# Optimization experiments

Hardware: AMD Instinct MI355X
Metric: run time of the kernel (lower is better)

Reference implementation:

```python
import jax, jax.numpy as jnp
import numpy as np

# Winograd F(2x2, 3x3) transform matrices
_BT = np.array([[1, 0, -1, 0],
                [0, 1,  1, 0],
                [0, -1, 1, 0],
                [0, 1,  0, -1]], dtype=np.float32)
_G = np.array([[1.0, 0.0, 0.0],
               [0.5, 0.5, 0.5],
               [0.5, -0.5, 0.5],
               [0.0, 0.0, 1.0]], dtype=np.float32)
_AT = np.array([[1, 1, 1, 0],
                [0, 1, -1, -1]], dtype=np.float32)


def setup_inputs() -> dict:
    key = jax.random.key(0)
    k1, k2, k3 = jax.random.split(key, 3)
    B, Cin, Cout, H, W = 16, 128, 256, 64, 64
    X = jax.random.normal(k1, (B, Cin, H, W), dtype=jnp.float32)
    # kaiming-uniform-ish scale for a 3x3 conv
    fan_in = Cin * 9
    bound = 1.0 / np.sqrt(fan_in)
    weight = jax.random.uniform(k2, (Cout, Cin, 3, 3), dtype=jnp.float32,
                                minval=-bound * np.sqrt(3.0), maxval=bound * np.sqrt(3.0))
    bias = jax.random.uniform(k3, (Cout,), dtype=jnp.float32, minval=-bound, maxval=bound)
    return {"X": X, "weight": weight, "bias": bias}


def reference(X, weight, bias):
    # Winograd F(2x2,3x3) convolution, stride 1, padding 1 ('same').
    BT = jnp.asarray(_BT, X.dtype)
    G = jnp.asarray(_G, X.dtype)
    AT = jnp.asarray(_AT, X.dtype)
    Bn, C, H, W = X.shape
    K = weight.shape[0]
    tH, tW = H // 2, W // 2  # number of 2x2 output tiles per dim

    xp = jnp.pad(X, ((0, 0), (0, 0), (1, 1), (1, 1)))
    # overlapping 4x4 input tiles with stride 2 -> [B, C, tH, tW, 4, 4]
    rows = (jnp.arange(tH) * 2)[:, None] + jnp.arange(4)[None, :]  # [tH,4]
    cols = (jnp.arange(tW) * 2)[:, None] + jnp.arange(4)[None, :]  # [tW,4]
    d = xp[:, :, rows[:, None, :, None], cols[None, :, None, :]]   # [B,C,tH,tW,4,4]

    # input transform V = B^T d B
    V = jnp.einsum('px,bcijxy,qy->bcijpq', BT, d, BT)
    # filter transform U = G g G^T -> [K,C,4,4]
    U = jnp.einsum('px,kcxy,qy->kcpq', G, weight, G)
    # elementwise product in transform domain, contracted over input channels
    M = jnp.einsum('kcpq,bcijpq->bkijpq', U, V)
    # inverse transform Y = A^T M A -> 2x2 output tiles
    Y = jnp.einsum('px,bkijxy,qy->bkijpq', AT, M, AT)  # [B,K,tH,tW,2,2]

    out = Y.transpose(0, 1, 2, 4, 3, 5).reshape(Bn, K, H, W)
    return out + bias[None, :, None, None]
```

## Files before the change

### kernel.cpp

```cpp
#include <hip/hip_runtime.h>
#include <hip/hip_bf16.h>
#include <cstdint>

#define CIN   128
#define COUT  256
#define BATCH 16
#define HH    64
#define WW    64
#define TH    32
#define TW    32
#define NT    (BATCH*TH*TW)
#define APQ   (COUT*CIN)
#define BPQ   (NT*CIN)

typedef __bf16 bf16x8 __attribute__((ext_vector_type(8)));
typedef float  f32x4  __attribute__((ext_vector_type(4)));

__device__ __forceinline__ void gload16(const void* g, void* l) {
    __builtin_amdgcn_global_load_lds(
        (const __attribute__((address_space(1))) uint32_t*)g,
        (__attribute__((address_space(3))) uint32_t*)l, 16, 0, 0);
}

__global__ __launch_bounds__(256) void wg_wtrans(const float* __restrict__ w,
                                                 __hip_bfloat16* __restrict__ U) {
    int idx = blockIdx.x * 256 + threadIdx.x;
    if (idx >= COUT * CIN) return;
    const float* wp = w + idx * 9;
    float g[3][3];
#pragma unroll
    for (int x = 0; x < 3; x++)
#pragma unroll
        for (int y = 0; y < 3; y++) g[x][y] = wp[x * 3 + y];

    float t[4][3];
#pragma unroll
    for (int y = 0; y < 3; y++) {
        t[0][y] = g[0][y];
        t[1][y] = 0.5f * (g[0][y] + g[1][y] + g[2][y]);
        t[2][y] = 0.5f * (g[0][y] - g[1][y] + g[2][y]);
        t[3][y] = g[2][y];
    }
#pragma unroll
    for (int p = 0; p < 4; p++) {
        float u0 = t[p][0];
        float u1 = 0.5f * (t[p][0] + t[p][1] + t[p][2]);
        float u2 = 0.5f * (t[p][0] - t[p][1] + t[p][2]);
        float u3 = t[p][2];
        U[(p * 4 + 0) * APQ + idx] = __float2bfloat16(u0);
        U[(p * 4 + 1) * APQ + idx] = __float2bfloat16(u1);
        U[(p * 4 + 2) * APQ + idx] = __float2bfloat16(u2);
        U[(p * 4 + 3) * APQ + idx] = __float2bfloat16(u3);
    }
}

__global__ __launch_bounds__(1024) void wg_itrans(const float* __restrict__ X,
                                                  __hip_bfloat16* __restrict__ V) {
    __shared__ float lds[32 * 265];
    const int c0 = blockIdx.x * 32;
    const int i  = blockIdx.y;
    const int b  = blockIdx.z;
    const int tid = threadIdx.x;

    for (int t = tid; t < 32 * 4; t += 1024) {
        int cc = t >> 2, r = t & 3;
        lds[cc * 265 + r * 66 + 0]  = 0.f;
        lds[cc * 265 + r * 66 + 65] = 0.f;
    }
    for (int t = tid; t < 32 * 4 * 64; t += 1024) {
        int x = t & 63, r = (t >> 6) & 3, cc = t >> 8;
        int y = 2 * i - 1 + r;
        float v = 0.f;
        if (y >= 0 && y < HH) v = X[(((b * CIN) + (c0 + cc)) * HH + y) * WW + x];
        lds[cc * 265 + r * 66 + 1 + x] = v;
    }
    __syncthreads();

    const int c = tid & 31;
    const int j = tid >> 5;
    const float* base = &lds[c * 265 + 2 * j];

    float t0[4], t1[4], t2[4], t3[4];
#pragma unroll
    for (int y = 0; y < 4; y++) {
        float a  = base[0 * 66 + y];
        float bb = base[1 * 66 + y];
        float cc = base[2 * 66 + y];
        float dd = base[3 * 66 + y];
        t0[y] = a - cc;
        t1[y] = bb + cc;
        t2[y] = cc - bb;
        t3[y] = bb - dd;
    }
    float vm[4][4];
#pragma unroll
    for (int p = 0; p < 4; p++) {
        const float* tp = (p == 0) ? t0 : (p == 1) ? t1 : (p == 2) ? t2 : t3;
        vm[p][0] = tp[0] - tp[2];
        vm[p][1] = tp[1] + tp[2];
        vm[p][2] = tp[2] - tp[1];
        vm[p][3] = tp[1] - tp[3];
    }

    const int bij = b * (TH * TW) + i * TW + j;
    const int vo  = bij * CIN + (c0 + c);
#pragma unroll
    for (int p = 0; p < 4; p++)
#pragma unroll
        for (int q = 0; q < 4; q++)
            V[(size_t)(p * 4 + q) * BPQ + vo] = __float2bfloat16(vm[p][q]);
}

#define ABYTES 16384
#define BUFSZ  32768

__global__ __launch_bounds__(512, 2) void wg_gemm6(const __hip_bfloat16* __restrict__ U,
                                                   const __hip_bfloat16* __restrict__ V,
                                                   const float* __restrict__ bias,
                                                   float* __restrict__ out) {
    __shared__ char lds[4 * BUFSZ];

    int orig = blockIdx.x;
    int wg   = (orig & 7) * 32 + (orig >> 3);
    const int mt = wg & 1, nt = wg >> 1;
    const int m0 = mt * 128, n0 = nt * 128;

    const int tid  = threadIdx.x;
    const int lane = tid & 63;
    const int wave = tid >> 6;
    const int wm = wave >> 2, wn = wave & 3;

    const __hip_bfloat16* pa[2];
    const __hip_bfloat16* pb[2];
    int ldsA[2], ldsB[2];
#pragma unroll
    for (int ch = 0; ch < 2; ch++) {
        int c = ch * 512 + tid;
        int R = c >> 3;
        int G = (c & 7) ^ (R & 7);
        pa[ch] = U + (m0 + R) * CIN + G * 8;
        pb[ch] = V + (size_t)(n0 + R) * CIN + G * 8;
        ldsA[ch] = c * 16;
        ldsB[ch] = ABYTES + c * 16;
    }

    auto stage = [&](int t, int buf) {
        const int pq = t >> 1;
        const int kb = (t & 1) * 64;
        char* base = lds + buf * BUFSZ;
        gload16(pa[0] + pq * APQ + kb, base + ldsA[0]);
        gload16(pa[1] + pq * APQ + kb, base + ldsA[1]);
        gload16(pb[0] + (size_t)pq * BPQ + kb, base + ldsB[0]);
        gload16(pb[1] + (size_t)pq * BPQ + kb, base + ldsB[1]);
    };

    const int la = lane & 15, hq = lane >> 4, l7 = lane & 7;
    int aoff[2], boff[2];
#pragma unroll
    for (int kk = 0; kk < 2; kk++) {
        int g = (kk * 4 + hq) ^ l7;
        aoff[kk] = (wm * 64 + la) * 128 + (g << 4);
        boff[kk] = ABYTES + (wn * 32 + la) * 128 + (g << 4);
    }

    f32x4 yac[2][2][4][2];
#pragma unroll
    for (int x = 0; x < 2; x++)
#pragma unroll
        for (int y = 0; y < 2; y++)
#pragma unroll
            for (int mi = 0; mi < 4; mi++)
#pragma unroll
                for (int nj = 0; nj < 2; nj++) yac[x][y][mi][nj] = (f32x4){0.f, 0.f, 0.f, 0.f};
    f32x4 mac[4][2];
    const f32x4 fz = (f32x4){0.f, 0.f, 0.f, 0.f};

    stage(0, 0);
    stage(1, 1);
    stage(2, 2);

#pragma unroll
    for (int t = 0; t < 32; ++t) {
        const int cur = t & 3;

        if (t <= 29)      asm volatile("s_waitcnt vmcnt(8)" ::: "memory");
        else if (t == 30) asm volatile("s_waitcnt vmcnt(4)" ::: "memory");
        else              asm volatile("s_waitcnt vmcnt(0)" ::: "memory");
        __builtin_amdgcn_s_barrier();
        __builtin_amdgcn_sched_barrier(0);

        if (t <= 28) stage(t + 3, (t + 3) & 3);

        const char* base = lds + cur * BUFSZ;
        bf16x8 av[4][2], bv[2][2];
#pragma unroll
        for (int mi = 0; mi < 4; mi++)
#pragma unroll
            for (int kk = 0; kk < 2; kk++)
                av[mi][kk] = *reinterpret_cast<const bf16x8*>(base + aoff[kk] + mi * 2048);
#pragma unroll
        for (int nj = 0; nj < 2; nj++)
#pragma unroll
            for (int kk = 0; kk < 2; kk++)
                bv[nj][kk] = *reinterpret_cast<const bf16x8*>(base + boff[kk] + nj * 2048);

        __builtin_amdgcn_s_setprio(1);
#pragma unroll
        for (int kk = 0; kk < 2; kk++)
#pragma unroll
            for (int mi = 0; mi < 4; mi++)
#pragma unroll
                for (int nj = 0; nj < 2; nj++)
                    mac[mi][nj] = __builtin_amdgcn_mfma_f32_16x16x32_bf16(
                        av[mi][kk], bv[nj][kk],
                        ((t & 1) == 0 && kk == 0) ? fz : mac[mi][nj], 0, 0, 0);
        __builtin_amdgcn_s_setprio(0);

        if (t & 1) {
            const int pq = t >> 1;
            const int p = pq >> 2, q = pq & 3;
            constexpr float W0[4] = {1.f, 1.f, 1.f, 0.f};
            constexpr float W1[4] = {0.f, 1.f, -1.f, -1.f};
            const float w00 = W0[p] * W0[q], w01 = W0[p] * W1[q];
            const float w10 = W1[p] * W0[q], w11 = W1[p] * W1[q];
#pragma unroll
            for (int mi = 0; mi < 4; mi++)
#pragma unroll
                for (int nj = 0; nj < 2; nj++) {
                    if (w00 != 0.f) yac[0][0][mi][nj] += w00 * mac[mi][nj];
                    if (w01 != 0.f) yac[0][1][mi][nj] += w01 * mac[mi][nj];
                    if (w10 != 0.f) yac[1][0][mi][nj] += w10 * mac[mi][nj];
                    if (w11 != 0.f) yac[1][1][mi][nj] += w11 * mac[mi][nj];
                }
        }
    }

    const int lr = lane & 15, rg = lane >> 4;
#pragma unroll
    for (int mi = 0; mi < 4; mi++) {
#pragma unroll
        for (int r = 0; r < 4; r++) {
            const int kout = m0 + wm * 64 + mi * 16 + rg * 4 + r;
            const float bvv = bias[kout];
#pragma unroll
            for (int nj = 0; nj < 2; nj++) {
                const int bij = n0 + wn * 32 + nj * 16 + lr;
                const int bb = bij >> 10, ti = (bij >> 5) & 31, tj = bij & 31;
                float* op = out + (((size_t)bb * COUT + kout) * HH + 2 * ti) * WW + 2 * tj;
                *reinterpret_cast<float2*>(op) =
                    make_float2(yac[0][0][mi][nj][r] + bvv, yac[0][1][mi][nj][r] + bvv);
                *reinterpret_cast<float2*>(op + WW) =
                    make_float2(yac[1][0][mi][nj][r] + bvv, yac[1][1][mi][nj][r] + bvv);
            }
        }
    }
}

extern "C" void kernel_launch(void* const* d_in, const int* in_sizes, int n_in,
                              void* d_out, int out_size, void* d_ws, size_t ws_size,
                              hipStream_t stream) {
    const float* X    = (const float*)d_in[0];
    const float* w    = (const float*)d_in[1];
    const float* bias = (const float*)d_in[2];
    float* out        = (float*)d_out;

    __hip_bfloat16* U = (__hip_bfloat16*)d_ws;
    __hip_bfloat16* V = (__hip_bfloat16*)((char*)d_ws + (1u << 20));

    wg_wtrans<<<(COUT * CIN + 255) / 256, 256, 0, stream>>>(w, U);
    wg_itrans<<<dim3(CIN / 32, TH, BATCH), 1024, 0, stream>>>(X, V);
    wg_gemm6<<<(COUT / 128) * (NT / 128), 512, 0, stream>>>(U, V, bias, out);
}
```

Measured before the change: 71.58 us.

## Split GEMM main loop into half-K phases with interleaved loads and barriers

Restructures the Winograd GEMM main loop into per-half-K phases. Each phase issues one chunk of global-to-LDS prefetch, reads its LDS fragments, waits and barriers, then runs a smaller batch of MFMAs, in the style of a ping-pong schedule. The loop is no longer fully unrolled, and the output-transform fold is rewritten to use runtime weight selects with unconditional multiply-adds. The aim is finer-grained overlap of memory and MFMA work. The cost is twice as many barriers per step and extra FMAs in the fold, since zero weights are no longer skipped.

```diff
diff --git a/kernel.cpp b/kernel.cpp
--- a/kernel.cpp
+++ b/kernel.cpp
@@ -114,7 +114,7 @@
 #define ABYTES 16384
 #define BUFSZ  32768
 
-__global__ __launch_bounds__(512, 2) void wg_gemm6(const __hip_bfloat16* __restrict__ U,
+__global__ __launch_bounds__(512, 2) void wg_gemm7(const __hip_bfloat16* __restrict__ U,
                                                    const __hip_bfloat16* __restrict__ V,
                                                    const float* __restrict__ bias,
                                                    float* __restrict__ out) {
@@ -144,16 +144,6 @@
         ldsB[ch] = ABYTES + c * 16;
     }
 
-    auto stage = [&](int t, int buf) {
-        const int pq = t >> 1;
-        const int kb = (t & 1) * 64;
-        char* base = lds + buf * BUFSZ;
-        gload16(pa[0] + pq * APQ + kb, base + ldsA[0]);
-        gload16(pa[1] + pq * APQ + kb, base + ldsA[1]);
-        gload16(pb[0] + (size_t)pq * BPQ + kb, base + ldsB[0]);
-        gload16(pb[1] + (size_t)pq * BPQ + kb, base + ldsB[1]);
-    };
-
     const int la = lane & 15, hq = lane >> 4, l7 = lane & 7;
     int aoff[2], boff[2];
 #pragma unroll
@@ -175,65 +165,85 @@
     f32x4 mac[4][2];
     const f32x4 fz = (f32x4){0.f, 0.f, 0.f, 0.f};
 
-    stage(0, 0);
-    stage(1, 1);
-    stage(2, 2);
-
-#pragma unroll
-    for (int t = 0; t < 32; ++t) {
-        const int cur = t & 3;
-
-        if (t <= 29)      asm volatile("s_waitcnt vmcnt(8)" ::: "memory");
-        else if (t == 30) asm volatile("s_waitcnt vmcnt(4)" ::: "memory");
-        else              asm volatile("s_waitcnt vmcnt(0)" ::: "memory");
+    auto ph = [&](int t, int kk, bool do_stage, bool init, int vmc) {
+        if (do_stage) {
+            const int ts = t + 3;
+            char* sb = lds + (ts & 3) * BUFSZ;
+            const int pq = ts >> 1, kb = (ts & 1) * 64;
+            gload16(pa[kk] + pq * APQ + kb, sb + ldsA[kk]);
+            gload16(pb[kk] + (size_t)pq * BPQ + kb, sb + ldsB[kk]);
+        }
+        const char* rb = lds + (t & 3) * BUFSZ;
+        bf16x8 av[4], bw[2];
+#pragma unroll
+        for (int mi = 0; mi < 4; mi++)
+            av[mi] = *reinterpret_cast<const bf16x8*>(rb + aoff[kk] + mi * 2048);
+#pragma unroll
+        for (int nj = 0; nj < 2; nj++)
+            bw[nj] = *reinterpret_cast<const bf16x8*>(rb + boff[kk] + nj * 2048);
+        __builtin_amdgcn_sched_barrier(0);
+        if (vmc == 8)      asm volatile("s_waitcnt vmcnt(8)");
+        else if (vmc == 4) asm volatile("s_waitcnt vmcnt(4)");
+        else if (vmc == 0) asm volatile("s_waitcnt vmcnt(0)");
         __builtin_amdgcn_s_barrier();
+        asm volatile("s_waitcnt lgkmcnt(0)");
         __builtin_amdgcn_sched_barrier(0);
-
-        if (t <= 28) stage(t + 3, (t + 3) & 3);
-
-        const char* base = lds + cur * BUFSZ;
-        bf16x8 av[4][2], bv[2][2];
+        __builtin_amdgcn_s_setprio(1);
 #pragma unroll
         for (int mi = 0; mi < 4; mi++)
 #pragma unroll
-            for (int kk = 0; kk < 2; kk++)
-                av[mi][kk] = *reinterpret_cast<const bf16x8*>(base + aoff[kk] + mi * 2048);
-#pragma unroll
-        for (int nj = 0; nj < 2; nj++)
-#pragma unroll
-            for (int kk = 0; kk < 2; kk++)
-                bv[nj][kk] = *reinterpret_cast<const bf16x8*>(base + boff[kk] + nj * 2048);
-
-        __builtin_amdgcn_s_setprio(1);
-#pragma unroll
-        for (int kk = 0; kk < 2; kk++)
-#pragma unroll
-            for (int mi = 0; mi < 4; mi++)
-#pragma unroll
-                for (int nj = 0; nj < 2; nj++)
-                    mac[mi][nj] = __builtin_amdgcn_mfma_f32_16x16x32_bf16(
-                        av[mi][kk], bv[nj][kk],
-                        ((t & 1) == 0 && kk == 0) ? fz : mac[mi][nj], 0, 0, 0);
+            for (int nj = 0; nj < 2; nj++)
+                mac[mi][nj] = __builtin_amdgcn_mfma_f32_16x16x32_bf16(
+                    av[mi], bw[nj], init ? fz : mac[mi][nj], 0, 0, 0);
         __builtin_amdgcn_s_setprio(0);
-
-        if (t & 1) {
-            const int pq = t >> 1;
-            const int p = pq >> 2, q = pq & 3;
-            constexpr float W0[4] = {1.f, 1.f, 1.f, 0.f};
-            constexpr float W1[4] = {0.f, 1.f, -1.f, -1.f};
-            const float w00 = W0[p] * W0[q], w01 = W0[p] * W1[q];
-            const float w10 = W1[p] * W0[q], w11 = W1[p] * W1[q];
-#pragma unroll
-            for (int mi = 0; mi < 4; mi++)
-#pragma unroll
-                for (int nj = 0; nj < 2; nj++) {
-                    if (w00 != 0.f) yac[0][0][mi][nj] += w00 * mac[mi][nj];
-                    if (w01 != 0.f) yac[0][1][mi][nj] += w01 * mac[mi][nj];
-                    if (w10 != 0.f) yac[1][0][mi][nj] += w10 * mac[mi][nj];
-                    if (w11 != 0.f) yac[1][1][mi][nj] += w11 * mac[mi][nj];
-                }
+        __builtin_amdgcn_sched_barrier(0);
+        __builtin_amdgcn_s_barrier();
+    };
+
+    auto fold = [&](int pq) {
+        const int p = pq >> 2, q = pq & 3;
+        const float w0p = (p == 3) ? 0.f : 1.f;
+        const float w1p = (p == 0) ? 0.f : ((p == 1) ? 1.f : -1.f);
+        const float w0q = (q == 3) ? 0.f : 1.f;
+        const float w1q = (q == 0) ? 0.f : ((q == 1) ? 1.f : -1.f);
+#pragma unroll
+        for (int mi = 0; mi < 4; mi++)
+#pragma unroll
+            for (int nj = 0; nj < 2; nj++) {
+                f32x4 m  = mac[mi][nj];
+                f32x4 q0 = w0q * m, q1 = w1q * m;
+                yac[0][0][mi][nj] += w0p * q0;
+                yac[0][1][mi][nj] += w0p * q1;
+                yac[1][0][mi][nj] += w1p * q0;
+                yac[1][1][mi][nj] += w1p * q1;
+            }
+    };
+
+    auto stage_full = [&](int t) {
+        char* sb = lds + (t & 3) * BUFSZ;
+        const int pq = t >> 1, kb = (t & 1) * 64;
+#pragma unroll
+        for (int ch = 0; ch < 2; ch++) {
+            gload16(pa[ch] + pq * APQ + kb, sb + ldsA[ch]);
+            gload16(pb[ch] + (size_t)pq * BPQ + kb, sb + ldsB[ch]);
         }
-    }
+    };
+
+    stage_full(0); stage_full(1); stage_full(2);
+    asm volatile("s_waitcnt vmcnt(8)");
+    __builtin_amdgcn_s_barrier();
+
+    for (int t = 0; t < 28; t += 2) {
+        ph(t,     0, true, true,  -1);
+        ph(t,     1, true, false,  8);
+        ph(t + 1, 0, true, false, -1);
+        ph(t + 1, 1, true, false,  8);
+        fold(t >> 1);
+    }
+    ph(28, 0, true,  true,  -1); ph(28, 1, true,  false, 8);
+    ph(29, 0, false, false, -1); ph(29, 1, false, false, 4); fold(14);
+    ph(30, 0, false, true,  -1); ph(30, 1, false, false, 0);
+    ph(31, 0, false, false, -1); ph(31, 1, false, false, -1); fold(15);
 
     const int lr = lane & 15, rg = lane >> 4;
 #pragma unroll
@@ -269,5 +279,5 @@
 
     wg_wtrans<<<(COUT * CIN + 255) / 256, 256, 0, stream>>>(w, U);
     wg_itrans<<<dim3(CIN / 32, TH, BATCH), 1024, 0, stream>>>(X, V);
-    wg_gemm6<<<(COUT / 128) * (NT / 128), 512, 0, stream>>>(U, V, bias, out);
-}
+    wg_gemm7<<<(COUT / 128) * (NT / 128), 512, 0, stream>>>(U, V, bias, out);
+}
```

Measured after the change: 70.01 us. 1.02x faster.
